# Kernel tuning notes

Measured on AMD Instinct MI355X. Metric: run time of the kernel, lower is better.

The kernel has to match this reference:

```python
import jax, jax.numpy as jnp
import numpy as np

NEG_INF = -9e15
ALPHA = 0.2  # leaky relu negative slope
N, M, F_IN, F_OUT = 20000, 64, 64, 64


def setup_inputs() -> dict:
    key = jax.random.key(0)
    k1, k2, k3, k4, k5 = jax.random.split(key, 5)
    item_embs = jax.random.normal(k1, (N, F_IN), dtype=jnp.float32)
    entity_embs = jax.random.normal(k2, (N, M, F_IN), dtype=jnp.float32)
    adj = jax.random.randint(k3, (N, M), 0, 2, dtype=jnp.int32)
    # xavier_uniform with gain=1.414
    def xavier(k, shape, gain=1.414):
        fan_in, fan_out = shape[0], shape[1]
        limit = gain * np.sqrt(6.0 / (fan_in + fan_out))
        return jax.random.uniform(k, shape, jnp.float32, -limit, limit)
    W = xavier(k4, (F_IN, F_OUT))
    a = xavier(k5, (2 * F_OUT, 1))
    return {"item_embs": item_embs, "entity_embs": entity_embs, "adj": adj, "W": W, "a": a}


def reference(item_embs, entity_embs, adj, W, a):
    # Dropouts are identity (inference mode).
    Wh = item_embs @ W                                   # [N, H]
    We = jnp.einsum('nmf,fh->nmh', entity_embs, W)       # [N, M, H]
    # cat(Wh, We) @ a  ==  Wh @ a[:H]  +  We @ a[H:]
    H = W.shape[1]
    a1, a2 = a[:H, 0], a[H:, 0]
    e = (Wh @ a1)[:, None] + We @ a2                     # [N, M]
    e = jax.nn.leaky_relu(e, negative_slope=ALPHA)
    e = jnp.where(adj > 0, e, NEG_INF)
    attention = jax.nn.softmax(e, axis=1)                # [N, M]
    # weighted aggregation of ORIGINAL entity embeddings + residual
    entity_weighted = jnp.einsum('nm,nmf->nf', attention, entity_embs)
    h_prime = entity_weighted + item_embs                # [N, F_IN]
    return h_prime  # concat=False -> no elu
```

## Files before the change

kernel.cpp:

```cpp
#include <hip/hip_runtime.h>

#define NEG_INF -9000000000000000.0f
#define ALPHA 0.2f

__global__ void precompute_wa(const float* __restrict__ W, const float* __restrict__ a,
                              float* __restrict__ wa) {
    __shared__ float a_sh[128];
    int t = threadIdx.x;
    a_sh[t] = a[t];
    __syncthreads();
    if (t < 64) {
        float s1 = 0.f, s2 = 0.f;
        const float* row = W + t * 64;
#pragma unroll
        for (int h = 0; h < 64; ++h) {
            float w = row[h];
            s1 += w * a_sh[h];
            s2 += w * a_sh[64 + h];
        }
        wa[t] = s1;
        wa[64 + t] = s2;
    }
}

__global__ __launch_bounds__(256) void gat_kernel(
    const float* __restrict__ item, const float* __restrict__ ent_g,
    const int* __restrict__ adj, const float* __restrict__ wa,
    float* __restrict__ out)
{
    constexpr int LDSTRIDE = 68;
    __shared__ float ent[64 * LDSTRIDE];
    __shared__ float wa1_sh[64];
    __shared__ float wa2_sh[64];
    __shared__ float item_sh[64];
    __shared__ float e_sh[64];
    __shared__ float red_sh[256];
    __shared__ float s1_sh;

    const int n = blockIdx.x;
    const int t = threadIdx.x;

    if (t < 64)       wa1_sh[t]        = wa[t];
    else if (t < 128) wa2_sh[t - 64]   = wa[t];
    else if (t < 192) item_sh[t - 128] = item[(size_t)n * 64 + (t - 128)];
    __syncthreads();

    if (t < 64) {
        float p = item_sh[t] * wa1_sh[t];
#pragma unroll
        for (int k = 1; k < 64; k <<= 1) p += __shfl_xor(p, k);
        if (t == 0) s1_sh = p;
    }

    const int m = t >> 2;
    const int q = t & 3;
    const float4* src = (const float4*)(ent_g + (size_t)n * 4096 + t * 16);
    float* dst = &ent[m * LDSTRIDE + q * 16];
    float partial = 0.f;
#pragma unroll
    for (int i = 0; i < 4; ++i) {
        float4 v = src[i];
        ((float4*)dst)[i] = v;
        const int c = q * 16 + i * 4;
        partial += v.x * wa2_sh[c]     + v.y * wa2_sh[c + 1]
                 + v.z * wa2_sh[c + 2] + v.w * wa2_sh[c + 3];
    }
    partial += __shfl_xor(partial, 1);
    partial += __shfl_xor(partial, 2);
    if (q == 0) e_sh[m] = partial;
    __syncthreads();

    if (t < 64) {
        float e = s1_sh + e_sh[t];
        e = e > 0.f ? e : ALPHA * e;
        if (adj[(size_t)n * 64 + t] <= 0) e = NEG_INF;
        float mx = e;
#pragma unroll
        for (int k = 1; k < 64; k <<= 1) mx = fmaxf(mx, __shfl_xor(mx, k));
        float ex = __expf(e - mx);
        float sm = ex;
#pragma unroll
        for (int k = 1; k < 64; k <<= 1) sm += __shfl_xor(sm, k);
        e_sh[t] = ex / sm;
    }
    __syncthreads();

    const int f = t & 63;
    const int g = t >> 6;
    float acc = 0.f;
#pragma unroll
    for (int mm = 0; mm < 16; ++mm) {
        const int row = g * 16 + mm;
        acc += e_sh[row] * ent[row * LDSTRIDE + f];
    }
    red_sh[t] = acc;
    __syncthreads();
    if (t < 64) {
        float o = red_sh[t] + red_sh[64 + t] + red_sh[128 + t] + red_sh[192 + t] + item_sh[t];
        out[(size_t)n * 64 + t] = o;
    }
}

extern "C" void kernel_launch(void* const* d_in, const int* in_sizes, int n_in,
                              void* d_out, int out_size, void* d_ws, size_t ws_size,
                              hipStream_t stream) {
    const float* item = (const float*)d_in[0];
    const float* ent  = (const float*)d_in[1];
    const int*   adj  = (const int*)d_in[2];
    const float* W    = (const float*)d_in[3];
    const float* a    = (const float*)d_in[4];
    float* out = (float*)d_out;
    float* wa  = (float*)d_ws;

    const int N = in_sizes[0] / 64;

    precompute_wa<<<1, 128, 0, stream>>>(W, a, wa);
    gat_kernel<<<N, 256, 0, stream>>>(item, ent, adj, wa, out);
}
```

Before: 441.1 us.

## Coalesce entity loads, issue global loads before first barrier, drop a sync

Entity rows are now loaded as fully coalesced float4 strides (each thread reads element i*256+t) instead of 16 contiguous floats per thread. The global loads for entities, adj and item are all issued up front. The first __syncthreads that staged wa into shared memory is removed, with wa read directly from global into registers. The per-row dot product now reduces across 16 lanes, and the LDS tile drops its padding to match the new layout. The goal is more memory-level parallelism and one fewer barrier per block, at the cost of more shuffles.

```diff
diff --git a/kernel.cpp b/kernel.cpp
--- a/kernel.cpp
+++ b/kernel.cpp
@@ -28,10 +28,7 @@
     const int* __restrict__ adj, const float* __restrict__ wa,
     float* __restrict__ out)
 {
-    constexpr int LDSTRIDE = 68;
-    __shared__ float ent[64 * LDSTRIDE];
-    __shared__ float wa1_sh[64];
-    __shared__ float wa2_sh[64];
+    __shared__ float ent[64 * 64];
     __shared__ float item_sh[64];
     __shared__ float e_sh[64];
     __shared__ float red_sh[256];
@@ -40,40 +37,44 @@
     const int n = blockIdx.x;
     const int t = threadIdx.x;
 
-    if (t < 64)       wa1_sh[t]        = wa[t];
-    else if (t < 128) wa2_sh[t - 64]   = wa[t];
-    else if (t < 192) item_sh[t - 128] = item[(size_t)n * 64 + (t - 128)];
-    __syncthreads();
+    const float4* src4 = (const float4*)(ent_g + (size_t)n * 4096);
+    float4 v[4];
+#pragma unroll
+    for (int i = 0; i < 4; ++i) v[i] = src4[i * 256 + t];
+
+    const int q = t & 15;
+    const float4 w2 = ((const float4*)(wa + 64))[q];
+    int adjv = 0;
+    float p1 = 0.f;
+    if (t < 64) {
+        adjv = adj[(size_t)n * 64 + t];
+        p1 = item[(size_t)n * 64 + t] * wa[t];
+    } else if (t < 128) {
+        item_sh[t - 64] = item[(size_t)n * 64 + (t - 64)];
+    }
+
+#pragma unroll
+    for (int i = 0; i < 4; ++i) {
+        ((float4*)ent)[i * 256 + t] = v[i];
+        float p = v[i].x * w2.x + v[i].y * w2.y + v[i].z * w2.z + v[i].w * w2.w;
+        p += __shfl_xor(p, 1);
+        p += __shfl_xor(p, 2);
+        p += __shfl_xor(p, 4);
+        p += __shfl_xor(p, 8);
+        if (q == 0) e_sh[i * 16 + (t >> 4)] = p;
+    }
 
     if (t < 64) {
-        float p = item_sh[t] * wa1_sh[t];
 #pragma unroll
-        for (int k = 1; k < 64; k <<= 1) p += __shfl_xor(p, k);
-        if (t == 0) s1_sh = p;
+        for (int k = 1; k < 64; k <<= 1) p1 += __shfl_xor(p1, k);
+        if (t == 0) s1_sh = p1;
     }
-
-    const int m = t >> 2;
-    const int q = t & 3;
-    const float4* src = (const float4*)(ent_g + (size_t)n * 4096 + t * 16);
-    float* dst = &ent[m * LDSTRIDE + q * 16];
-    float partial = 0.f;
-#pragma unroll
-    for (int i = 0; i < 4; ++i) {
-        float4 v = src[i];
-        ((float4*)dst)[i] = v;
-        const int c = q * 16 + i * 4;
-        partial += v.x * wa2_sh[c]     + v.y * wa2_sh[c + 1]
-                 + v.z * wa2_sh[c + 2] + v.w * wa2_sh[c + 3];
-    }
-    partial += __shfl_xor(partial, 1);
-    partial += __shfl_xor(partial, 2);
-    if (q == 0) e_sh[m] = partial;
     __syncthreads();
 
     if (t < 64) {
         float e = s1_sh + e_sh[t];
         e = e > 0.f ? e : ALPHA * e;
-        if (adj[(size_t)n * 64 + t] <= 0) e = NEG_INF;
+        if (adjv <= 0) e = NEG_INF;
         float mx = e;
 #pragma unroll
         for (int k = 1; k < 64; k <<= 1) mx = fmaxf(mx, __shfl_xor(mx, k));
@@ -91,13 +92,13 @@
 #pragma unroll
     for (int mm = 0; mm < 16; ++mm) {
         const int row = g * 16 + mm;
-        acc += e_sh[row] * ent[row * LDSTRIDE + f];
+        acc += e_sh[row] * ent[row * 64 + f];
     }
     red_sh[t] = acc;
     __syncthreads();
     if (t < 64) {
-        float o = red_sh[t] + red_sh[64 + t] + red_sh[128 + t] + red_sh[192 + t] + item_sh[t];
-        out[(size_t)n * 64 + t] = o;
+        out[(size_t)n * 64 + t] =
+            red_sh[t] + red_sh[64 + t] + red_sh[128 + t] + red_sh[192 + t] + item_sh[t];
     }
 }
 
```

Result: no change. 438.6 us (-0.6%).
